# Performance work log

Measured on AMD Instinct MI355X. Metric: run time of the kernel, lower is better.

The kernel has to match this reference:

```python
import jax, jax.numpy as jnp
import numpy as np

WS = 8          # window_size
NH = 8          # num_heads
DIM = 256
HD = DIM // NH  # head_dim = 32
HID = DIM * 4   # mlp hidden = 1024
EPS = 1e-5


def _rel_pos_index(ws):
    coords = np.stack(np.meshgrid(np.arange(ws), np.arange(ws), indexing='ij'))  # [2,ws,ws]
    cf = coords.reshape(2, -1)                              # [2, ws*ws]
    rel = cf[:, :, None] - cf[:, None, :]                   # [2, N, N]
    rel = rel.transpose(1, 2, 0)                            # [N, N, 2]
    rel[:, :, 0] += ws - 1
    rel[:, :, 1] += ws - 1
    rel[:, :, 0] *= 2 * ws - 1
    return jnp.asarray(rel.sum(-1))                          # [N, N] int

REL_IDX = _rel_pos_index(WS)


def _layernorm(x, g, b):
    mu = jnp.mean(x, axis=-1, keepdims=True)
    var = jnp.mean((x - mu) ** 2, axis=-1, keepdims=True)
    return (x - mu) * jax.lax.rsqrt(var + EPS) * g + b


def setup_inputs() -> dict:
    key = jax.random.key(0)
    ks = jax.random.split(key, 10)
    B, H, Wd, C = 4, 256, 256, DIM
    x = jax.random.normal(ks[0], (B, H * Wd, C), dtype=jnp.float32)
    s = 0.02
    return {
        'x': x,
        'ln1_g': jnp.ones((C,), jnp.float32),
        'ln1_b': jnp.zeros((C,), jnp.float32),
        'qkv_w': jax.random.normal(ks[1], (C, 3 * C), jnp.float32) * s,
        'qkv_b': jnp.zeros((3 * C,), jnp.float32),
        'proj_w': jax.random.normal(ks[2], (C, C), jnp.float32) * s,
        'proj_b': jnp.zeros((C,), jnp.float32),
        'bias_table': jax.random.normal(ks[3], ((2 * WS - 1) ** 2, NH), jnp.float32) * s,
        'ln2_g': jnp.ones((C,), jnp.float32),
        'ln2_b': jnp.zeros((C,), jnp.float32),
        'fc1_w': jax.random.normal(ks[4], (C, HID), jnp.float32) * s,
        'fc1_b': jnp.zeros((HID,), jnp.float32),
        'fc2_w': jax.random.normal(ks[5], (HID, C), jnp.float32) * s,
        'fc2_b': jnp.zeros((C,), jnp.float32),
        'H': H,
        'W': Wd,
    }


def _window_attention(xw, qkv_w, qkv_b, proj_w, proj_b, bias_table):
    # xw: [B_, N, C] with N = WS*WS
    B_, N, C = xw.shape
    qkv = (xw @ qkv_w + qkv_b).reshape(B_, N, 3, NH, HD)
    q, k, v = qkv[:, :, 0], qkv[:, :, 1], qkv[:, :, 2]      # [B_, N, NH, HD]
    scale = HD ** -0.5
    attn = jnp.einsum('bnhd,bmhd->bhnm', q, k) * scale       # [B_, NH, N, N]
    bias = bias_table[REL_IDX.reshape(-1)].reshape(N, N, NH).transpose(2, 0, 1)
    attn = jax.nn.softmax(attn + bias[None], axis=-1)
    out = jnp.einsum('bhnm,bmhd->bnhd', attn, v).reshape(B_, N, C)
    return out @ proj_w + proj_b


def reference(x, ln1_g, ln1_b, qkv_w, qkv_b, proj_w, proj_b, bias_table,
              ln2_g, ln2_b, fc1_w, fc1_b, fc2_w, fc2_b, H, W):
    B, L, C = x.shape
    shortcut = x
    h = _layernorm(x, ln1_g, ln1_b).reshape(B, H, W, C)
    pad_r = (WS - W % WS) % WS
    pad_b = (WS - H % WS) % WS
    if pad_r or pad_b:
        h = jnp.pad(h, ((0, 0), (0, pad_b), (0, pad_r), (0, 0)))
    Hp, Wp = h.shape[1], h.shape[2]
    # window partition -> [B*nW, WS*WS, C]
    h = h.reshape(B, Hp // WS, WS, Wp // WS, WS, C).transpose(0, 1, 3, 2, 4, 5)
    h = h.reshape(-1, WS * WS, C)
    h = _window_attention(h, qkv_w, qkv_b, proj_w, proj_b, bias_table)
    # window reverse
    h = h.reshape(B, Hp // WS, Wp // WS, WS, WS, C).transpose(0, 1, 3, 2, 4, 5)
    h = h.reshape(B, Hp, Wp, C)
    if pad_r or pad_b:
        h = h[:, :H, :W, :]
    h = shortcut + h.reshape(B, H * W, C)
    m = _layernorm(h, ln2_g, ln2_b)
    m = jax.nn.gelu(m @ fc1_w + fc1_b, approximate=False) @ fc2_w + fc2_b
    return h + m
```

## Files before the change

kernel.cpp:

```cpp
#include <hip/hip_runtime.h>
#include <hip/hip_bf16.h>
#include <math.h>

typedef __attribute__((ext_vector_type(8))) short short8;
typedef __attribute__((ext_vector_type(4))) float f32x4;

__device__ __forceinline__ unsigned short f2bf(float f){
  union { __hip_bfloat16 h; unsigned short u; } cv;
  cv.h = __float2bfloat16(f);
  return cv.u;
}

__device__ __forceinline__ float bf2f(unsigned short u){
  union { unsigned int i; float f; } v;
  v.i = ((unsigned int)u) << 16;
  return v.f;
}

__device__ __forceinline__ unsigned char f2fp8(float v){
  return (unsigned char)(__builtin_amdgcn_cvt_pk_fp8_f32(v, v, 0, 0) & 0xff);
}

__device__ __forceinline__ float gelu_f(float v){
  float v2 = v * v;
  float nw = v * fmaf(-0.10294364f, v2, -2.3022090f);
  float e  = __builtin_amdgcn_exp2f(nw);
  return v * __builtin_amdgcn_rcpf(1.f + e);
}

__device__ __forceinline__ void gload_lds16(const void* g, void* l){
  __builtin_amdgcn_global_load_lds(
      (const __attribute__((address_space(1))) void*)g,
      (__attribute__((address_space(3))) void*)l, 16, 0, 0);
}

__global__ __launch_bounds__(256) void wconv4(
    const float* __restrict__ qkv_w, const float* __restrict__ proj_w,
    const float* __restrict__ fc1_w, const float* __restrict__ fc2_w,
    unsigned char* __restrict__ wq, unsigned short* __restrict__ wp,
    unsigned char* __restrict__ w1, unsigned char* __restrict__ w2){
  int idx = blockIdx.x * 256 + threadIdx.x;
  if (idx < 196608){
    int k = idx / 768, n = idx % 768;
    wq[n*256 + k] = f2fp8(qkv_w[idx] * 64.f);
  } else if (idx < 262144){
    int l = idx - 196608;
    int k = l >> 8, n = l & 255;
    wp[n*256 + k] = f2bf(proj_w[l]);
  } else if (idx < 524288){
    int l = idx - 262144;
    int k = l >> 10, n = l & 1023;
    w1[n*256 + k] = f2fp8(fc1_w[l] * 64.f);
  } else {
    int l = idx - 524288;
    int k = l >> 8, n = l & 255;
    w2[n*1024 + k] = f2fp8(fc2_w[l] * 64.f);
  }
}

__global__ __launch_bounds__(256) void ln_kernel(
    const float* __restrict__ x, const float* __restrict__ g,
    const float* __restrict__ b, unsigned char* __restrict__ out){
  const int lane = threadIdx.x & 63;
  const int wv = threadIdx.x >> 6;
  const long row = (long)blockIdx.x * 4 + wv;
  const float4 xv = ((const float4*)(x + row * 256))[lane];
  float s  = xv.x + xv.y + xv.z + xv.w;
  float s2 = xv.x*xv.x + xv.y*xv.y + xv.z*xv.z + xv.w*xv.w;
  #pragma unroll
  for (int m = 1; m < 64; m <<= 1){
    s  += __shfl_xor(s,  m);
    s2 += __shfl_xor(s2, m);
  }
  float mu = s * (1.f/256.f);
  float rs = rsqrtf(s2 * (1.f/256.f) - mu*mu + 1e-5f);
  float4 gv = ((const float4*)g)[lane];
  float4 bv = ((const float4*)b)[lane];
  float v0 = 16.f * ((xv.x - mu)*rs*gv.x + bv.x);
  float v1 = 16.f * ((xv.y - mu)*rs*gv.y + bv.y);
  float v2 = 16.f * ((xv.z - mu)*rs*gv.z + bv.z);
  float v3 = 16.f * ((xv.w - mu)*rs*gv.w + bv.w);
  int p = __builtin_amdgcn_cvt_pk_fp8_f32(v0, v1, 0, 0);
  p = __builtin_amdgcn_cvt_pk_fp8_f32(v2, v3, p, 1);
  ((unsigned int*)(out + row * 256))[lane] = (unsigned int)p;
}

template<int MODE>
__global__ __launch_bounds__(256, 4) void gemm_fp8(
    const unsigned char* __restrict__ A,
    const unsigned char* __restrict__ Bt,
    const float* __restrict__ bias,
    const unsigned short* __restrict__ res,
    void* __restrict__ out,
    int N, int K, int nbx, float sc){
  __shared__ unsigned char S[2*128*128];
  unsigned char* As = S;
  unsigned char* Bs = S + 128*128;
  const int tid  = threadIdx.x;
  const int lane = tid & 63;
  const int wave = tid >> 6;
  const int wm = wave >> 1, wn = wave & 1;

  const int nby  = gridDim.x / nbx;
  const int bid  = blockIdx.x;
  const int xcd  = bid & 7;
  const int local = bid >> 3;
  const int lrow = local / nbx;
  const int rowb = xcd * (nby >> 3) + lrow;
  const int colb = local - lrow * nbx;
  const long row0 = (long)rowb * 128;
  const int  col0 = colb * 128;
  const int l15 = lane & 15, l4 = lane >> 4;

  f32x4 acc[4][4];
  #pragma unroll
  for (int i = 0; i < 4; ++i)
    #pragma unroll
    for (int j = 0; j < 4; ++j)
      acc[i][j] = (f32x4){0.f, 0.f, 0.f, 0.f};

  const int nk = K >> 7;
  for (int kt = 0; kt < nk; ++kt){
    #pragma unroll
    for (int it = 0; it < 4; ++it){
      int ch = it*256 + tid;
      int r = ch >> 3, cc = ch & 7;
      int srcc = ((cc ^ (r & 7)) << 4);
      gload_lds16(A  + (row0 + r) * K + kt*128 + srcc, &As[ch*16]);
      gload_lds16(Bt + (long)(col0 + r) * K + kt*128 + srcc, &Bs[ch*16]);
    }
    __syncthreads();
    #pragma unroll
    for (int ks = 0; ks < 4; ++ks){
      long af[4], bfr[4];
      #pragma unroll
      for (int mi = 0; mi < 4; ++mi){
        int ar = wm*64 + mi*16 + l15;
        af[mi] = *(const long*)&As[ar*128 + (((2*ks + (l4 >> 1)) ^ (ar & 7)) << 4) + 8*(l4 & 1)];
      }
      #pragma unroll
      for (int ni = 0; ni < 4; ++ni){
        int br = wn*64 + ni*16 + l15;
        bfr[ni] = *(const long*)&Bs[br*128 + (((2*ks + (l4 >> 1)) ^ (br & 7)) << 4) + 8*(l4 & 1)];
      }
      #pragma unroll
      for (int mi = 0; mi < 4; ++mi)
        #pragma unroll
        for (int ni = 0; ni < 4; ++ni)
          acc[mi][ni] = __builtin_amdgcn_mfma_f32_16x16x32_fp8_fp8(bfr[ni], af[mi], acc[mi][ni], 0, 0, 0);
    }
    __syncthreads();
  }

  if (MODE == 2){
    float* outf = (float*)out;
    #pragma unroll
    for (int mi = 0; mi < 4; ++mi){
      long row = row0 + wm*64 + mi*16 + l15;
      #pragma unroll
      for (int ni = 0; ni < 4; ++ni){
        int colg = col0 + wn*64 + ni*16 + 4*l4;
        float4 bv = *(const float4*)&bias[colg];
        long idx = row * N + colg;
        ushort4 rv = *(const ushort4*)&res[idx];
        float4 o;
        o.x = acc[mi][ni][0]*sc + bv.x + bf2f(rv.x);
        o.y = acc[mi][ni][1]*sc + bv.y + bf2f(rv.y);
        o.z = acc[mi][ni][2]*sc + bv.z + bf2f(rv.z);
        o.w = acc[mi][ni][3]*sc + bv.w + bf2f(rv.w);
        *(float4*)&outf[idx] = o;
      }
    }
  } else if (MODE == 1){
    unsigned char* outp = (unsigned char*)out;
    #pragma unroll
    for (int mi = 0; mi < 4; ++mi){
      long row = row0 + wm*64 + mi*16 + l15;
      #pragma unroll
      for (int ni = 0; ni < 4; ++ni){
        int colg = col0 + wn*64 + ni*16 + 4*l4;
        float4 bv = *(const float4*)&bias[colg];
        float v0 = 8.f * gelu_f(acc[mi][ni][0]*sc + bv.x);
        float v1 = 8.f * gelu_f(acc[mi][ni][1]*sc + bv.y);
        float v2 = 8.f * gelu_f(acc[mi][ni][2]*sc + bv.z);
        float v3 = 8.f * gelu_f(acc[mi][ni][3]*sc + bv.w);
        int p = __builtin_amdgcn_cvt_pk_fp8_f32(v0, v1, 0, 0);
        p = __builtin_amdgcn_cvt_pk_fp8_f32(v2, v3, p, 1);
        *(unsigned int*)&outp[row * N + colg] = (unsigned int)p;
      }
    }
  } else {
    unsigned short* outp = (unsigned short*)out;
    #pragma unroll
    for (int mi = 0; mi < 4; ++mi){
      long row = row0 + wm*64 + mi*16 + l15;
      #pragma unroll
      for (int ni = 0; ni < 4; ++ni){
        int colg = col0 + wn*64 + ni*16 + 4*l4;
        float4 bv = *(const float4*)&bias[colg];
        uint2 dv;
        dv.x = ((unsigned int)f2bf(acc[mi][ni][1]*sc + bv.y) << 16) | f2bf(acc[mi][ni][0]*sc + bv.x);
        dv.y = ((unsigned int)f2bf(acc[mi][ni][3]*sc + bv.w) << 16) | f2bf(acc[mi][ni][2]*sc + bv.z);
        *(uint2*)&outp[row * N + colg] = dv;
      }
    }
  }
}

__global__ __launch_bounds__(64, 3) void attn_kernel(
    const unsigned short* __restrict__ qkv,
    const float* __restrict__ bt,
    unsigned short* __restrict__ ao){
  __shared__ unsigned short P[64*64];
  const int lane = threadIdx.x;
  const int wb = blockIdx.x;
  const int w = wb >> 3, h = wb & 7;
  const int bidx = w >> 10, rem = w & 1023;
  const int wy = rem >> 5, wx = rem & 31;
  const long tok0 = (long)bidx * 65536 + (long)wy * 2048 + wx * 8;
  const int l15 = lane & 15, l4 = lane >> 4;

  short8 qf[4], kf[4];
  #pragma unroll
  for (int t = 0; t < 4; ++t){
    int n = t*16 + l15;
    long tok = tok0 + (n >> 3) * 256 + (n & 7);
    qf[t] = *(const short8*)(qkv + tok*768 +       h*32 + 8*l4);
    kf[t] = *(const short8*)(qkv + tok*768 + 256 + h*32 + 8*l4);
  }
  f32x4 s[4][4];
  #pragma unroll
  for (int i = 0; i < 4; ++i)
    #pragma unroll
    for (int j = 0; j < 4; ++j)
      s[i][j] = (f32x4){0.f, 0.f, 0.f, 0.f};
  #pragma unroll
  for (int mi = 0; mi < 4; ++mi)
    #pragma unroll
    for (int ni = 0; ni < 4; ++ni)
      s[mi][ni] = __builtin_amdgcn_mfma_f32_16x16x32_bf16(kf[ni], qf[mi], s[mi][ni], 0, 0, 0);

  const float scale = 0.17677669529663687f;
  #pragma unroll
  for (int mi = 0; mi < 4; ++mi){
    int q = mi*16 + l15;
    int ny = q >> 3, nx = q & 7;
    #pragma unroll
    for (int ni = 0; ni < 4; ++ni){
      #pragma unroll
      for (int j = 0; j < 4; ++j){
        int k = ni*16 + 4*l4 + j;
        int db = (ny - (k >> 3) + 7) * 15 + (nx - (k & 7) + 7);
        s[mi][ni][j] = s[mi][ni][j] * scale + bt[db*8 + h];
      }
    }
    float mx = -1e30f;
    #pragma unroll
    for (int ni = 0; ni < 4; ++ni)
      #pragma unroll
      for (int j = 0; j < 4; ++j)
        mx = fmaxf(mx, s[mi][ni][j]);
    mx = fmaxf(mx, __shfl_xor(mx, 16));
    mx = fmaxf(mx, __shfl_xor(mx, 32));
    float sm = 0.f;
    #pragma unroll
    for (int ni = 0; ni < 4; ++ni)
      #pragma unroll
      for (int j = 0; j < 4; ++j){
        float p = __expf(s[mi][ni][j] - mx);
        s[mi][ni][j] = p;
        sm += p;
      }
    sm += __shfl_xor(sm, 16);
    sm += __shfl_xor(sm, 32);
    float inv = __builtin_amdgcn_rcpf(sm);
    #pragma unroll
    for (int ni = 0; ni < 4; ++ni){
      uint2 dv;
      dv.x = ((unsigned int)f2bf(s[mi][ni][1]*inv) << 16) | f2bf(s[mi][ni][0]*inv);
      dv.y = ((unsigned int)f2bf(s[mi][ni][3]*inv) << 16) | f2bf(s[mi][ni][2]*inv);
      int g = ni*2 + (l4 >> 1);
      *(uint2*)&P[q*64 + ((g ^ (q & 7)) << 3) + 4*(l4 & 1)] = dv;
    }
  }

  f32x4 o[4][2];
  #pragma unroll
  for (int i = 0; i < 4; ++i)
    #pragma unroll
    for (int j = 0; j < 2; ++j)
      o[i][j] = (f32x4){0.f, 0.f, 0.f, 0.f};
  #pragma unroll
  for (int kt = 0; kt < 2; ++kt){
    short8 vf[2];
    #pragma unroll
    for (int ni = 0; ni < 2; ++ni){
      union { unsigned short u[8]; short8 v; } tmp;
      #pragma unroll
      for (int i = 0; i < 8; ++i){
        int kk = kt*32 + 8*l4 + i;
        long tok = tok0 + (kk >> 3) * 256 + (kk & 7);
        tmp.u[i] = qkv[tok*768 + 512 + h*32 + ni*16 + l15];
      }
      vf[ni] = tmp.v;
    }
    #pragma unroll
    for (int mi = 0; mi < 4; ++mi){
      int r = mi*16 + l15;
      short8 pf = *(const short8*)&P[r*64 + (((kt*4 + l4) ^ (r & 7)) << 3)];
      #pragma unroll
      for (int ni = 0; ni < 2; ++ni)
        o[mi][ni] = __builtin_amdgcn_mfma_f32_16x16x32_bf16(vf[ni], pf, o[mi][ni], 0, 0, 0);
    }
  }
  #pragma unroll
  for (int mi = 0; mi < 4; ++mi){
    int t = mi*16 + l15;
    long tok = tok0 + (t >> 3) * 256 + (t & 7);
    #pragma unroll
    for (int ni = 0; ni < 2; ++ni){
      uint2 dv;
      dv.x = ((unsigned int)f2bf(o[mi][ni][1]) << 16) | f2bf(o[mi][ni][0]);
      dv.y = ((unsigned int)f2bf(o[mi][ni][3]) << 16) | f2bf(o[mi][ni][2]);
      *(uint2*)&ao[tok*256 + h*32 + ni*16 + 4*l4] = dv;
    }
  }
}

__global__ __launch_bounds__(512, 4) void proj_ln2(
    const unsigned short* __restrict__ A,
    const unsigned short* __restrict__ Bt,
    const float* __restrict__ bias,
    const float* __restrict__ res,
    const float* __restrict__ g2,
    const float* __restrict__ b2,
    unsigned short* __restrict__ hout,
    unsigned char* __restrict__ hn){
  __shared__ unsigned short As[128*64];
  __shared__ unsigned short Bs[256*64];
  __shared__ float redsum[4][128];
  __shared__ float redsq[4][128];
  __shared__ float mu_s[128];
  __shared__ float rs_s[128];
  const int tid = threadIdx.x, lane = tid & 63, wave = tid >> 6;
  const int l15 = lane & 15, l4 = lane >> 4;
  const int wm = wave >> 2, wn = wave & 3;
  const long row0 = (long)blockIdx.x * 128;

  f32x4 acc[4][4];
  #pragma unroll
  for (int i = 0; i < 4; ++i)
    #pragma unroll
    for (int j = 0; j < 4; ++j)
      acc[i][j] = (f32x4){0.f, 0.f, 0.f, 0.f};

  for (int kt = 0; kt < 4; ++kt){
    #pragma unroll
    for (int it = 0; it < 2; ++it){
      int ch = it*512 + tid;
      int r = ch >> 3, cc = ch & 7;
      gload_lds16(A + (row0 + r)*256 + kt*64 + ((cc ^ (r & 7))*8), &As[ch*8]);
    }
    #pragma unroll
    for (int it = 0; it < 4; ++it){
      int ch = it*512 + tid;
      int r = ch >> 3, cc = ch & 7;
      gload_lds16(Bt + r*256 + kt*64 + ((cc ^ (r & 7))*8), &Bs[ch*8]);
    }
    __syncthreads();
    #pragma unroll
    for (int ks = 0; ks < 2; ++ks){
      short8 af[4], bf[4];
      #pragma unroll
      for (int mi = 0; mi < 4; ++mi){
        int ar = wm*64 + mi*16 + l15;
        af[mi] = *(const short8*)&As[ar*64 + (((ks*4 + l4) ^ (ar & 7))*8)];
      }
      #pragma unroll
      for (int ni = 0; ni < 4; ++ni){
        int br = wn*64 + ni*16 + l15;
        bf[ni] = *(const short8*)&Bs[br*64 + (((ks*4 + l4) ^ (br & 7))*8)];
      }
      #pragma unroll
      for (int mi = 0; mi < 4; ++mi)
        #pragma unroll
        for (int ni = 0; ni < 4; ++ni)
          acc[mi][ni] = __builtin_amdgcn_mfma_f32_16x16x32_bf16(af[mi], bf[ni], acc[mi][ni], 0, 0, 0);
    }
    __syncthreads();
  }

  float bcol[4];
  #pragma unroll
  for (int ni = 0; ni < 4; ++ni) bcol[ni] = bias[wn*64 + ni*16 + l15];
  f32x4 psum[4], psq[4];
  #pragma unroll
  for (int mi = 0; mi < 4; ++mi){
    psum[mi] = (f32x4){0.f,0.f,0.f,0.f};
    psq[mi]  = (f32x4){0.f,0.f,0.f,0.f};
    #pragma unroll
    for (int ni = 0; ni < 4; ++ni){
      int col = wn*64 + ni*16 + l15;
      #pragma unroll
      for (int j = 0; j < 4; ++j){
        long row = row0 + wm*64 + mi*16 + 4*l4 + j;
        long idx = row * 256 + col;
        float v = acc[mi][ni][j] + bcol[ni] + res[idx];
        hout[idx] = f2bf(v);
        acc[mi][ni][j] = v;
        psum[mi][j] += v;
        psq[mi][j]  += v * v;
      }
    }
  }
  #pragma unroll
  for (int mi = 0; mi < 4; ++mi){
    #pragma unroll
    for (int j = 0; j < 4; ++j){
      float s = psum[mi][j], q = psq[mi][j];
      #pragma unroll
      for (int m = 1; m < 16; m <<= 1){
        s += __shfl_xor(s, m);
        q += __shfl_xor(q, m);
      }
      if (l15 == 0){
        int rl = wm*64 + mi*16 + 4*l4 + j;
        redsum[wn][rl] = s;
        redsq[wn][rl]  = q;
      }
    }
  }
  __syncthreads();
  if (tid < 128){
    float s = redsum[0][tid] + redsum[1][tid] + redsum[2][tid] + redsum[3][tid];
    float q = redsq[0][tid]  + redsq[1][tid]  + redsq[2][tid]  + redsq[3][tid];
    float mu = s * (1.f/256.f);
    mu_s[tid] = mu;
    rs_s[tid] = rsqrtf(q * (1.f/256.f) - mu*mu + 1e-5f);
  }
  __syncthreads();
  float gcol[4], b2col[4];
  #pragma unroll
  for (int ni = 0; ni < 4; ++ni){
    gcol[ni]  = g2[wn*64 + ni*16 + l15];
    b2col[ni] = b2[wn*64 + ni*16 + l15];
  }
  #pragma unroll
  for (int mi = 0; mi < 4; ++mi){
    #pragma unroll
    for (int j = 0; j < 4; ++j){
      int rl = wm*64 + mi*16 + 4*l4 + j;
      float mu = mu_s[rl], rs = rs_s[rl];
      long row = row0 + rl;
      #pragma unroll
      for (int ni = 0; ni < 4; ++ni){
        int col = wn*64 + ni*16 + l15;
        hn[row*256 + col] = f2fp8(16.f * ((acc[mi][ni][j] - mu)*rs*gcol[ni] + b2col[ni]));
      }
    }
  }
}

extern "C" void kernel_launch(void* const* d_in, const int* in_sizes, int n_in,
                              void* d_out, int out_size, void* d_ws, size_t ws_size,
                              hipStream_t stream){
  const float* x      = (const float*)d_in[0];
  const float* ln1_g  = (const float*)d_in[1];
  const float* ln1_b  = (const float*)d_in[2];
  const float* qkv_w  = (const float*)d_in[3];
  const float* qkv_b  = (const float*)d_in[4];
  const float* proj_w = (const float*)d_in[5];
  const float* proj_b = (const float*)d_in[6];
  const float* btab   = (const float*)d_in[7];
  const float* ln2_g  = (const float*)d_in[8];
  const float* ln2_b  = (const float*)d_in[9];
  const float* fc1_w  = (const float*)d_in[10];
  const float* fc1_b  = (const float*)d_in[11];
  const float* fc2_w  = (const float*)d_in[12];
  const float* fc2_b  = (const float*)d_in[13];

  const long M = (long)in_sizes[0] / 256;

  char* ws = (char*)d_ws;
  unsigned char*  xn8  = (unsigned char*)(ws);
  unsigned short* ao   = (unsigned short*)(ws);
  unsigned char*  act8 = (unsigned char*)(ws);
  unsigned short* qkv  = (unsigned short*)(ws + 134217728);
  unsigned char*  hn8  = (unsigned char*)(ws + 536870912);
  unsigned char*  wqf8 = (unsigned char*)(ws + 671088640);
  unsigned short* wp   = (unsigned short*)(wqf8 + 196608);
  unsigned char*  w1f8 = (unsigned char*)(wp + 256*256);
  unsigned char*  w2f8 = w1f8 + 256*1024;
  unsigned short* hh   = (unsigned short*)(ws + (712ull << 20));
  float* outf = (float*)d_out;

  wconv4<<<3072, 256, 0, stream>>>(qkv_w, proj_w, fc1_w, fc2_w, wqf8, wp, w1f8, w2f8);

  ln_kernel<<<M/4, 256, 0, stream>>>(x, ln1_g, ln1_b, xn8);
  gemm_fp8<0><<<6 * (M/128), 256, 0, stream>>>(xn8, wqf8, qkv_b, nullptr, qkv, 768, 256, 6, 1.f/1024.f);
  attn_kernel<<<(M/64) * 8, 64, 0, stream>>>(qkv, btab, ao);
  proj_ln2<<<M/128, 512, 0, stream>>>(ao, wp, proj_b, x, ln2_g, ln2_b, hh, hn8);
  gemm_fp8<1><<<8 * (M/128), 256, 0, stream>>>(hn8, w1f8, fc1_b, nullptr, act8, 1024, 256, 8, 1.f/1024.f);
  gemm_fp8<2><<<2 * (M/128), 256, 0, stream>>>(act8, w2f8, fc2_b, hh, outf, 256, 1024, 2, 1.f/512.f);
}
```

Measured before the change: 1.057 ms.

## Store QKV as scaled FP8 and run window attention with FP8 MFMA

The QKV GEMM epilogue gains a mode that writes the projections as FP8 with a fixed x16 scale instead of bf16. The attention kernel loads these FP8 operands, computes QK^T and PV with fp8 MFMA, and keeps the softmax probabilities in a smaller padded FP8 shared buffer. Scales are undone in the softmax scale and the output write. This halves the QKV intermediate traffic and LDS footprint, at the cost of lower accuracy from FP8 quantization of Q, K, V and P, plus an added barrier.

```diff
diff --git a/kernel.cpp b/kernel.cpp
--- a/kernel.cpp
+++ b/kernel.cpp
@@ -171,7 +171,7 @@
         *(float4*)&outf[idx] = o;
       }
     }
-  } else if (MODE == 1){
+  } else if (MODE == 1 || MODE == 3){
     unsigned char* outp = (unsigned char*)out;
     #pragma unroll
     for (int mi = 0; mi < 4; ++mi){
@@ -180,10 +180,18 @@
       for (int ni = 0; ni < 4; ++ni){
         int colg = col0 + wn*64 + ni*16 + 4*l4;
         float4 bv = *(const float4*)&bias[colg];
-        float v0 = 8.f * gelu_f(acc[mi][ni][0]*sc + bv.x);
-        float v1 = 8.f * gelu_f(acc[mi][ni][1]*sc + bv.y);
-        float v2 = 8.f * gelu_f(acc[mi][ni][2]*sc + bv.z);
-        float v3 = 8.f * gelu_f(acc[mi][ni][3]*sc + bv.w);
+        float v0, v1, v2, v3;
+        if (MODE == 1){
+          v0 = 8.f * gelu_f(acc[mi][ni][0]*sc + bv.x);
+          v1 = 8.f * gelu_f(acc[mi][ni][1]*sc + bv.y);
+          v2 = 8.f * gelu_f(acc[mi][ni][2]*sc + bv.z);
+          v3 = 8.f * gelu_f(acc[mi][ni][3]*sc + bv.w);
+        } else {
+          v0 = 16.f * (acc[mi][ni][0]*sc + bv.x);
+          v1 = 16.f * (acc[mi][ni][1]*sc + bv.y);
+          v2 = 16.f * (acc[mi][ni][2]*sc + bv.z);
+          v3 = 16.f * (acc[mi][ni][3]*sc + bv.w);
+        }
         int p = __builtin_amdgcn_cvt_pk_fp8_f32(v0, v1, 0, 0);
         p = __builtin_amdgcn_cvt_pk_fp8_f32(v2, v3, p, 1);
         *(unsigned int*)&outp[row * N + colg] = (unsigned int)p;
@@ -208,10 +216,10 @@
 }
 
 __global__ __launch_bounds__(64, 3) void attn_kernel(
-    const unsigned short* __restrict__ qkv,
+    const unsigned char* __restrict__ qkv,
     const float* __restrict__ bt,
     unsigned short* __restrict__ ao){
-  __shared__ unsigned short P[64*64];
+  __shared__ unsigned int P8[64*18];
   const int lane = threadIdx.x;
   const int wb = blockIdx.x;
   const int w = wb >> 3, h = wb & 7;
@@ -220,13 +228,13 @@
   const long tok0 = (long)bidx * 65536 + (long)wy * 2048 + wx * 8;
   const int l15 = lane & 15, l4 = lane >> 4;
 
-  short8 qf[4], kf[4];
+  long qf[4], kf[4];
   #pragma unroll
   for (int t = 0; t < 4; ++t){
     int n = t*16 + l15;
     long tok = tok0 + (n >> 3) * 256 + (n & 7);
-    qf[t] = *(const short8*)(qkv + tok*768 +       h*32 + 8*l4);
-    kf[t] = *(const short8*)(qkv + tok*768 + 256 + h*32 + 8*l4);
+    qf[t] = *(const long*)(qkv + tok*768 +       h*32 + 8*l4);
+    kf[t] = *(const long*)(qkv + tok*768 + 256 + h*32 + 8*l4);
   }
   f32x4 s[4][4];
   #pragma unroll
@@ -238,9 +246,9 @@
   for (int mi = 0; mi < 4; ++mi)
     #pragma unroll
     for (int ni = 0; ni < 4; ++ni)
-      s[mi][ni] = __builtin_amdgcn_mfma_f32_16x16x32_bf16(kf[ni], qf[mi], s[mi][ni], 0, 0, 0);
-
-  const float scale = 0.17677669529663687f;
+      s[mi][ni] = __builtin_amdgcn_mfma_f32_16x16x32_fp8_fp8(kf[ni], qf[mi], s[mi][ni], 0, 0, 0);
+
+  const float scale = 0.17677669529663687f / 256.f;
   #pragma unroll
   for (int mi = 0; mi < 4; ++mi){
     int q = mi*16 + l15;
@@ -273,16 +281,15 @@
       }
     sm += __shfl_xor(sm, 16);
     sm += __shfl_xor(sm, 32);
-    float inv = __builtin_amdgcn_rcpf(sm);
+    float inv16 = 16.f * __builtin_amdgcn_rcpf(sm);
     #pragma unroll
     for (int ni = 0; ni < 4; ++ni){
-      uint2 dv;
-      dv.x = ((unsigned int)f2bf(s[mi][ni][1]*inv) << 16) | f2bf(s[mi][ni][0]*inv);
-      dv.y = ((unsigned int)f2bf(s[mi][ni][3]*inv) << 16) | f2bf(s[mi][ni][2]*inv);
-      int g = ni*2 + (l4 >> 1);
-      *(uint2*)&P[q*64 + ((g ^ (q & 7)) << 3) + 4*(l4 & 1)] = dv;
-    }
-  }
+      int p = __builtin_amdgcn_cvt_pk_fp8_f32(s[mi][ni][0]*inv16, s[mi][ni][1]*inv16, 0, 0);
+      p = __builtin_amdgcn_cvt_pk_fp8_f32(s[mi][ni][2]*inv16, s[mi][ni][3]*inv16, p, 1);
+      P8[q*18 + ni*4 + l4] = (unsigned int)p;
+    }
+  }
+  __syncthreads();
 
   f32x4 o[4][2];
   #pragma unroll
@@ -292,27 +299,31 @@
       o[i][j] = (f32x4){0.f, 0.f, 0.f, 0.f};
   #pragma unroll
   for (int kt = 0; kt < 2; ++kt){
-    short8 vf[2];
+    long vf[2];
     #pragma unroll
     for (int ni = 0; ni < 2; ++ni){
-      union { unsigned short u[8]; short8 v; } tmp;
+      union { unsigned char b[8]; long v; } tmp;
       #pragma unroll
       for (int i = 0; i < 8; ++i){
         int kk = kt*32 + 8*l4 + i;
         long tok = tok0 + (kk >> 3) * 256 + (kk & 7);
-        tmp.u[i] = qkv[tok*768 + 512 + h*32 + ni*16 + l15];
+        tmp.b[i] = qkv[tok*768 + 512 + h*32 + ni*16 + l15];
       }
       vf[ni] = tmp.v;
     }
     #pragma unroll
     for (int mi = 0; mi < 4; ++mi){
-      int r = mi*16 + l15;
-      short8 pf = *(const short8*)&P[r*64 + (((kt*4 + l4) ^ (r & 7)) << 3)];
+      int rr = mi*16 + l15;
+      union { unsigned int u[2]; long v; } pfu;
+      pfu.u[0] = P8[rr*18 + kt*8 + 2*l4];
+      pfu.u[1] = P8[rr*18 + kt*8 + 2*l4 + 1];
+      long pf = pfu.v;
       #pragma unroll
       for (int ni = 0; ni < 2; ++ni)
-        o[mi][ni] = __builtin_amdgcn_mfma_f32_16x16x32_bf16(vf[ni], pf, o[mi][ni], 0, 0, 0);
-    }
-  }
+        o[mi][ni] = __builtin_amdgcn_mfma_f32_16x16x32_fp8_fp8(vf[ni], pf, o[mi][ni], 0, 0, 0);
+    }
+  }
+  const float osc = 1.f / 256.f;
   #pragma unroll
   for (int mi = 0; mi < 4; ++mi){
     int t = mi*16 + l15;
@@ -320,8 +331,8 @@
     #pragma unroll
     for (int ni = 0; ni < 2; ++ni){
       uint2 dv;
-      dv.x = ((unsigned int)f2bf(o[mi][ni][1]) << 16) | f2bf(o[mi][ni][0]);
-      dv.y = ((unsigned int)f2bf(o[mi][ni][3]) << 16) | f2bf(o[mi][ni][2]);
+      dv.x = ((unsigned int)f2bf(o[mi][ni][1]*osc) << 16) | f2bf(o[mi][ni][0]*osc);
+      dv.y = ((unsigned int)f2bf(o[mi][ni][3]*osc) << 16) | f2bf(o[mi][ni][2]*osc);
       *(uint2*)&ao[tok*256 + h*32 + ni*16 + 4*l4] = dv;
     }
   }
@@ -485,7 +496,7 @@
   unsigned char*  xn8  = (unsigned char*)(ws);
   unsigned short* ao   = (unsigned short*)(ws);
   unsigned char*  act8 = (unsigned char*)(ws);
-  unsigned short* qkv  = (unsigned short*)(ws + 134217728);
+  unsigned char*  qkv8 = (unsigned char*)(ws + 335544320);
   unsigned char*  hn8  = (unsigned char*)(ws + 536870912);
   unsigned char*  wqf8 = (unsigned char*)(ws + 671088640);
   unsigned short* wp   = (unsigned short*)(wqf8 + 196608);
@@ -497,8 +508,8 @@
   wconv4<<<3072, 256, 0, stream>>>(qkv_w, proj_w, fc1_w, fc2_w, wqf8, wp, w1f8, w2f8);
 
   ln_kernel<<<M/4, 256, 0, stream>>>(x, ln1_g, ln1_b, xn8);
-  gemm_fp8<0><<<6 * (M/128), 256, 0, stream>>>(xn8, wqf8, qkv_b, nullptr, qkv, 768, 256, 6, 1.f/1024.f);
-  attn_kernel<<<(M/64) * 8, 64, 0, stream>>>(qkv, btab, ao);
+  gemm_fp8<3><<<6 * (M/128), 256, 0, stream>>>(xn8, wqf8, qkv_b, nullptr, qkv8, 768, 256, 6, 1.f/1024.f);
+  attn_kernel<<<(M/64) * 8, 64, 0, stream>>>(qkv8, btab, ao);
   proj_ln2<<<M/128, 512, 0, stream>>>(ao, wp, proj_b, x, ln2_g, ln2_b, hh, hn8);
   gemm_fp8<1><<<8 * (M/128), 256, 0, stream>>>(hn8, w1f8, fc1_b, nullptr, act8, 1024, 256, 8, 1.f/1024.f);
   gemm_fp8<2><<<2 * (M/128), 256, 0, stream>>>(act8, w2f8, fc2_b, hh, outf, 256, 1024, 2, 1.f/512.f);
```

After: 998.6 us. 1.06x faster.
